# Kernel optimization log

Measured on AMD Instinct MI355X. Metric: run time of the kernel, lower is better.

Reference implementation:

```python
import jax, jax.numpy as jnp
import numpy as np

DN = ('NCHW', 'OIHW', 'NCHW')

def _convlstm_scan(x, W, b):
    """x: [S,B,Cin,H,W]; W: [4*Co, Cin+Co, 3, 3]; b: [4*Co]. Returns all h: [S,B,Co,H,W]."""
    S, B, Cin, H, Wd = x.shape
    Co = W.shape[0] // 4
    h0 = jnp.zeros((B, Co, H, Wd), x.dtype)
    c0 = jnp.zeros((B, Co, H, Wd), x.dtype)

    def step(carry, xt):
        h, c = carry
        z = jax.lax.conv_general_dilated(
            jnp.concatenate([xt, h], axis=1), W,
            window_strides=(1, 1), padding='SAME', dimension_numbers=DN)
        z = z + b[None, :, None, None]
        i, f, o, g = jnp.split(z, 4, axis=1)
        c = jax.nn.sigmoid(f) * c + jax.nn.sigmoid(i) * jnp.tanh(g)
        h = jax.nn.sigmoid(o) * jnp.tanh(c)
        return (h, c), h

    _, outs = jax.lax.scan(step, (h0, c0), x)
    return outs


def setup_inputs() -> dict:
    key = jax.random.key(0)
    k1, k2, k3 = jax.random.split(key, 3)
    S, B, C, H, W = 16, 4, 32, 128, 128
    Co = 32
    x = jax.random.normal(k1, (S, B, C, H, W), dtype=jnp.float32)
    Wf = jax.random.normal(k2, (4 * Co, C + Co, 3, 3), dtype=jnp.float32) * 0.05
    bf = jnp.zeros((4 * Co,), dtype=jnp.float32)
    Wb = jax.random.normal(k3, (4 * Co, C + Co, 3, 3), dtype=jnp.float32) * 0.05
    bb = jnp.zeros((4 * Co,), dtype=jnp.float32)
    return {"x": x, "Wf": Wf, "bf": bf, "Wb": Wb, "bb": bb}


def reference(x, Wf, bf, Wb, bb):
    fwd_outs = _convlstm_scan(x, Wf, bf)            # [S,B,Co,H,W]
    bwd_outs = _convlstm_scan(x[::-1], Wb, bb)      # [S,B,Co,H,W] (time-reversed input)
    # Faithful to source: backward outputs concatenated WITHOUT re-flipping.
    return jnp.concatenate([fwd_outs, bwd_outs], axis=2)  # [S,B,2*Co,H,W]
```

## Files before the change

### kernel.cpp

```cpp
#include <hip/hip_runtime.h>

#define S_ 16
#define B_ 4
#define H_ 128
#define W_ 128
#define HW_ (H_ * W_)
#define NPOS 324
#define TILE_ELEMS (NPOS * 32)

typedef __attribute__((ext_vector_type(8))) _Float16 half8;
typedef __attribute__((ext_vector_type(4))) float f32x4;

__device__ __forceinline__ float sigf(float x) { return 1.f / (1.f + __expf(-x)); }
__device__ __forceinline__ float tanhf_(float x) { return 2.f / (1.f + __expf(-2.f * x)) - 1.f; }

__global__ void prep_pack(const float* __restrict__ Wf, const float* __restrict__ Wb,
                          _Float16* __restrict__ wpk) {
    int id = blockIdx.x * 256 + threadIdx.x;
    if (id >= 18432) return;
    int l = id & 63;
    int nf = (id >> 6) & 7;
    int ks = (id >> 9) % 18;
    int d = id / 9216;
    const float* Wsrc = d ? Wb : Wf;
    int tap = ks >> 1, half = ks & 1;
    int dy = tap / 3, dx = tap - dy * 3;
    int co = nf * 16 + (l & 15);
    _Float16* dst = wpk + (size_t)d * 73728 + ((size_t)(ks * 8 + nf) * 64 + l) * 8;
#pragma unroll
    for (int e = 0; e < 8; ++e) {
        int ci = half * 32 + (l >> 4) * 8 + e;
        dst[e] = (_Float16)Wsrc[((co * 64 + ci) * 3 + dy) * 3 + dx];
    }
}

__global__ void prep_xtiles(const float* __restrict__ x, _Float16* __restrict__ xt) {
    int id = blockIdx.x * 256 + threadIdx.x;
    if (id >= 16 * 4 * 64 * NPOS * 4) return;
    int cb = id & 3;
    int u = id >> 2;
    int pos = u % NPOS;
    int v = u / NPOS;
    int tile = v & 63;
    v >>= 6;
    int b = v & 3;
    int ts = v >> 2;
    int r = pos / 18, cc = pos - r * 18;
    int gy = (tile >> 3) * 16 + r - 1;
    int gx = (tile & 7) * 16 + cc - 1;
    bool inb = ((unsigned)gy < 128u) && ((unsigned)gx < 128u);
    const float* g = x + ((size_t)(ts * 4 + b) * 32 + cb * 8) * HW_ + (size_t)gy * W_ + gx;
    half8 vv;
#pragma unroll
    for (int e = 0; e < 8; ++e)
        vv[e] = inb ? (_Float16)g[e * HW_] : (_Float16)0.f;
    *(half8*)(xt + (size_t)u * 32 + cb * 8) = vv;
}

__device__ __forceinline__ half8 lda(const _Float16* __restrict__ base, int m, int dy,
                                     int dx, int px, int kg, int wq) {
    return *(const half8*)(base + (size_t)(((wq * 4 + m + dy) * 18) + px + dx) * 32 + kg * 8);
}
__device__ __forceinline__ half8 ldb(const _Float16* __restrict__ bw, int ks, int nf, int lane) {
    return *(const half8*)(bw + (size_t)(ks * 8 + nf) * 512 + lane * 8);
}

__global__ __launch_bounds__(256, 2)
void convlstm_step(const _Float16* __restrict__ xtiles,
                   const _Float16* __restrict__ hin,
                   _Float16* __restrict__ hout,
                   const _Float16* __restrict__ wpk,
                   const float* __restrict__ biasf, const float* __restrict__ biasb,
                   float* __restrict__ cst, float* __restrict__ out, int t) {
    const int tile = blockIdx.x;
    const int dirb = blockIdx.y;
    const int dir = dirb >> 2, b = dirb & 3;
    const int ts = dir ? (S_ - 1 - t) : t;

    const _Float16* base_x = xtiles + ((size_t)(ts * 4 + b) * 64 + tile) * TILE_ELEMS;
    const _Float16* base_h = hin + ((size_t)dirb * 64 + tile) * TILE_ELEMS;
    _Float16* hob = hout + (size_t)dirb * 64 * TILE_ELEMS;
    const _Float16* bw = wpk + (size_t)dir * 73728;
    const float* bias = dir ? biasb : biasf;
    float* cbase = cst + (size_t)dirb * 32 * HW_;
    float* outp = out + ((size_t)(t * 4 + b) * 64 + dir * 32) * HW_;

    const int tid = threadIdx.x;
    const int lane = tid & 63, wq = tid >> 6;
    const int px = lane & 15, kg = lane >> 4;

    f32x4 acc[4][8];
#pragma unroll
    for (int m = 0; m < 4; ++m)
#pragma unroll
        for (int nf = 0; nf < 8; ++nf) acc[m][nf] = (f32x4)(0.f);

    if (t == 0) {
#pragma unroll 1
        for (int tap = 0; tap < 9; ++tap) {
            int dy = tap / 3, dx = tap - dy * 3;
            half8 a[4];
#pragma unroll
            for (int m = 0; m < 4; ++m) a[m] = lda(base_x, m, dy, dx, px, kg, wq);
#pragma unroll
            for (int nf = 0; nf < 8; ++nf) {
                half8 bb8 = ldb(bw, tap * 2, nf, lane);
#pragma unroll
                for (int m = 0; m < 4; ++m)
                    acc[m][nf] = __builtin_amdgcn_mfma_f32_16x16x32_f16(a[m], bb8, acc[m][nf], 0, 0, 0);
            }
        }
    } else {
        half8 bcur[8], bnxt[8];
        half8 ax[4], ah[4];
#pragma unroll
        for (int nf = 0; nf < 8; ++nf) bcur[nf] = ldb(bw, 0, nf, lane);
        {
            int dy = 0, dx = 0;
#pragma unroll
            for (int m = 0; m < 4; ++m) ax[m] = lda(base_x, m, dy, dx, px, kg, wq);
        }
#pragma unroll 1
        for (int tap = 0; tap < 9; ++tap) {
            const int dy = tap / 3, dx = tap - dy * 3;
#pragma unroll
            for (int nf = 0; nf < 8; ++nf) bnxt[nf] = ldb(bw, tap * 2 + 1, nf, lane);
#pragma unroll
            for (int m = 0; m < 4; ++m) ah[m] = lda(base_h, m, dy, dx, px, kg, wq);
#pragma unroll
            for (int nf = 0; nf < 8; ++nf)
#pragma unroll
                for (int m = 0; m < 4; ++m)
                    acc[m][nf] = __builtin_amdgcn_mfma_f32_16x16x32_f16(ax[m], bcur[nf], acc[m][nf], 0, 0, 0);
            if (tap < 8) {
                const int tn = tap + 1;
                const int dy2 = tn / 3, dx2 = tn - dy2 * 3;
#pragma unroll
                for (int nf = 0; nf < 8; ++nf) bcur[nf] = ldb(bw, tn * 2, nf, lane);
#pragma unroll
                for (int m = 0; m < 4; ++m) ax[m] = lda(base_x, m, dy2, dx2, px, kg, wq);
            }
#pragma unroll
            for (int nf = 0; nf < 8; ++nf)
#pragma unroll
                for (int m = 0; m < 4; ++m)
                    acc[m][nf] = __builtin_amdgcn_mfma_f32_16x16x32_f16(ah[m], bnxt[nf], acc[m][nf], 0, 0, 0);
        }
    }

    const int q0 = px;
    const int gx0 = (tile & 7) * 16, gy0 = (tile >> 3) * 16;
    const int tx = tile & 7, ty_ = tile >> 3;
    const int lx0 = kg * 4;

    float bI[2], bF[2], bO[2], bG[2];
#pragma unroll
    for (int qs = 0; qs < 2; ++qs) {
        bI[qs] = bias[qs * 16 + q0];
        bF[qs] = bias[32 + qs * 16 + q0];
        bO[qs] = bias[64 + qs * 16 + q0];
        bG[qs] = bias[96 + qs * 16 + q0];
    }
#pragma unroll
    for (int m = 0; m < 4; ++m) {
        const int ly = wq * 4 + m;
        const int gy = gy0 + ly;
#pragma unroll
        for (int qs = 0; qs < 2; ++qs) {
            const int q = qs * 16 + q0;
            f32x4 zi = acc[m][qs], zf = acc[m][2 + qs], zo = acc[m][4 + qs], zg = acc[m][6 + qs];
            size_t off = (size_t)q * HW_ + (size_t)gy * W_ + gx0 + lx0;
            f32x4 cold = (f32x4)(0.f);
            if (t) cold = *(const f32x4*)(cbase + off);
            f32x4 cn, hn;
#pragma unroll
            for (int r = 0; r < 4; ++r) {
                float I = sigf(zi[r] + bI[qs]);
                float F = sigf(zf[r] + bF[qs]);
                float O = sigf(zo[r] + bO[qs]);
                float G = tanhf_(zg[r] + bG[qs]);
                float cnr = F * cold[r] + I * G;
                cn[r] = cnr;
                hn[r] = O * tanhf_(cnr);
            }
            *(f32x4*)(cbase + off) = cn;
            *(f32x4*)(outp + off) = hn;
#pragma unroll
            for (int r = 0; r < 4; ++r) {
                _Float16 hh = (_Float16)hn[r];
                int lx = lx0 + r;
                hob[((size_t)tile) * TILE_ELEMS + (size_t)((ly + 1) * 18 + lx + 1) * 32 + q] = hh;
                bool Le = (lx == 0) && (tx > 0);
                bool Re = (lx == 15) && (tx < 7);
                bool Te = (ly == 0) && (ty_ > 0);
                bool Be = (ly == 15) && (ty_ < 7);
                if (Le) hob[((size_t)tile - 1) * TILE_ELEMS + (size_t)((ly + 1) * 18 + 17) * 32 + q] = hh;
                if (Re) hob[((size_t)tile + 1) * TILE_ELEMS + (size_t)((ly + 1) * 18 + 0) * 32 + q] = hh;
                if (Te) hob[((size_t)tile - 8) * TILE_ELEMS + (size_t)(17 * 18 + lx + 1) * 32 + q] = hh;
                if (Be) hob[((size_t)tile + 8) * TILE_ELEMS + (size_t)(0 * 18 + lx + 1) * 32 + q] = hh;
                if (Te && Le) hob[((size_t)tile - 9) * TILE_ELEMS + (size_t)(17 * 18 + 17) * 32 + q] = hh;
                if (Te && Re) hob[((size_t)tile - 7) * TILE_ELEMS + (size_t)(17 * 18 + 0) * 32 + q] = hh;
                if (Be && Le) hob[((size_t)tile + 7) * TILE_ELEMS + (size_t)(0 * 18 + 17) * 32 + q] = hh;
                if (Be && Re) hob[((size_t)tile + 9) * TILE_ELEMS + (size_t)(0 * 18 + 0) * 32 + q] = hh;
            }
        }
    }
}

extern "C" void kernel_launch(void* const* d_in, const int* in_sizes, int n_in,
                              void* d_out, int out_size, void* d_ws, size_t ws_size,
                              hipStream_t stream) {
    const float* x  = (const float*)d_in[0];
    const float* Wf = (const float*)d_in[1];
    const float* bf = (const float*)d_in[2];
    const float* Wb = (const float*)d_in[3];
    const float* bb = (const float*)d_in[4];
    float* out = (float*)d_out;
    char* ws = (char*)d_ws;

    const size_t OFF_WPK = 0;
    const size_t OFF_XT  = 327680;
    const size_t OFF_H0  = OFF_XT + 84934656;
    const size_t OFF_H1  = OFF_H0 + 10616832;
    const size_t OFF_C   = OFF_H1 + 10616832;

    _Float16* wpk = (_Float16*)(ws + OFF_WPK);
    _Float16* xt  = (_Float16*)(ws + OFF_XT);
    _Float16* hb[2] = { (_Float16*)(ws + OFF_H0), (_Float16*)(ws + OFF_H1) };
    float* cst = (float*)(ws + OFF_C);

    hipMemsetAsync(ws + OFF_H0, 0, 2u * 10616832u, stream);

    prep_pack<<<dim3(72), dim3(256), 0, stream>>>(Wf, Wb, wpk);
    prep_xtiles<<<dim3(20736), dim3(256), 0, stream>>>(x, xt);

    for (int t = 0; t < S_; ++t) {
        convlstm_step<<<dim3(64, 8), dim3(256), 0, stream>>>(
            xt, hb[(t + 1) & 1], hb[t & 1], wpk, bf, bb, cst, out, t);
    }
}
```

Measured before the change: 660.0 us.

## Stage packed weights through double-buffered LDS via direct global-to-LDS loads

In the recurrent path, each wave used to load all eight weight fragments per k-step from global memory into registers. Now each wave loads two fragments per k-step directly into a double-buffered shared-memory tile with global_load_lds, and all waves read them back from LDS. A block barrier is added per k-step, and A-operand loads for the next step are software-pipelined. This cuts redundant global weight traffic and register pressure, at the cost of one __syncthreads per k-step and LDS reads.

```diff
diff --git a/kernel.cpp b/kernel.cpp
--- a/kernel.cpp
+++ b/kernel.cpp
@@ -13,6 +13,12 @@
 
 __device__ __forceinline__ float sigf(float x) { return 1.f / (1.f + __expf(-x)); }
 __device__ __forceinline__ float tanhf_(float x) { return 2.f / (1.f + __expf(-2.f * x)) - 1.f; }
+
+__device__ __forceinline__ void gl2lds16(const _Float16* g, _Float16* l) {
+    __builtin_amdgcn_global_load_lds(
+        (const __attribute__((address_space(1))) unsigned int*)g,
+        (__attribute__((address_space(3))) unsigned int*)l, 16, 0, 0);
+}
 
 __global__ void prep_pack(const float* __restrict__ Wf, const float* __restrict__ Wb,
                           _Float16* __restrict__ wpk) {
@@ -85,6 +91,8 @@
     float* cbase = cst + (size_t)dirb * 32 * HW_;
     float* outp = out + ((size_t)(t * 4 + b) * 64 + dir * 32) * HW_;
 
+    __shared__ alignas(16) _Float16 bsh[2][8][64][8];
+
     const int tid = threadIdx.x;
     const int lane = tid & 63, wq = tid >> 6;
     const int px = lane & 15, kg = lane >> 4;
@@ -111,40 +119,41 @@
             }
         }
     } else {
-        half8 bcur[8], bnxt[8];
-        half8 ax[4], ah[4];
-#pragma unroll
-        for (int nf = 0; nf < 8; ++nf) bcur[nf] = ldb(bw, 0, nf, lane);
+        half8 aP[4], aQ[4];
         {
-            int dy = 0, dx = 0;
-#pragma unroll
-            for (int m = 0; m < 4; ++m) ax[m] = lda(base_x, m, dy, dx, px, kg, wq);
-        }
+            const _Float16* gs = bw + ((size_t)(0 * 8 + wq * 2) * 64 + lane) * 8;
+            gl2lds16(gs, &bsh[0][wq * 2][0][0]);
+            gl2lds16(gs + 512, &bsh[0][wq * 2 + 1][0][0]);
+#pragma unroll
+            for (int m = 0; m < 4; ++m) aP[m] = lda(base_x, m, 0, 0, px, kg, wq);
+        }
+
+        auto body = [&](int ks, half8(&acur)[4], half8(&anxt)[4]) {
+            __syncthreads();
+            if (ks < 17) {
+                const int ksn = ks + 1;
+                const _Float16* gs = bw + ((size_t)(ksn * 8 + wq * 2) * 64 + lane) * 8;
+                gl2lds16(gs, &bsh[ksn & 1][wq * 2][0][0]);
+                gl2lds16(gs + 512, &bsh[ksn & 1][wq * 2 + 1][0][0]);
+                const int tapn = ksn >> 1;
+                const int dyn_ = tapn / 3, dxn = tapn - dyn_ * 3;
+                const _Float16* an = (ksn & 1) ? base_h : base_x;
+#pragma unroll
+                for (int m = 0; m < 4; ++m) anxt[m] = lda(an, m, dyn_, dxn, px, kg, wq);
+            }
+            const _Float16* lb = &bsh[ks & 1][0][0][0];
+#pragma unroll
+            for (int nf = 0; nf < 8; ++nf) {
+                half8 bb8 = *(const half8*)(lb + nf * 512 + lane * 8);
+#pragma unroll
+                for (int m = 0; m < 4; ++m)
+                    acc[m][nf] = __builtin_amdgcn_mfma_f32_16x16x32_f16(acur[m], bb8, acc[m][nf], 0, 0, 0);
+            }
+        };
 #pragma unroll 1
-        for (int tap = 0; tap < 9; ++tap) {
-            const int dy = tap / 3, dx = tap - dy * 3;
-#pragma unroll
-            for (int nf = 0; nf < 8; ++nf) bnxt[nf] = ldb(bw, tap * 2 + 1, nf, lane);
-#pragma unroll
-            for (int m = 0; m < 4; ++m) ah[m] = lda(base_h, m, dy, dx, px, kg, wq);
-#pragma unroll
-            for (int nf = 0; nf < 8; ++nf)
-#pragma unroll
-                for (int m = 0; m < 4; ++m)
-                    acc[m][nf] = __builtin_amdgcn_mfma_f32_16x16x32_f16(ax[m], bcur[nf], acc[m][nf], 0, 0, 0);
-            if (tap < 8) {
-                const int tn = tap + 1;
-                const int dy2 = tn / 3, dx2 = tn - dy2 * 3;
-#pragma unroll
-                for (int nf = 0; nf < 8; ++nf) bcur[nf] = ldb(bw, tn * 2, nf, lane);
-#pragma unroll
-                for (int m = 0; m < 4; ++m) ax[m] = lda(base_x, m, dy2, dx2, px, kg, wq);
-            }
-#pragma unroll
-            for (int nf = 0; nf < 8; ++nf)
-#pragma unroll
-                for (int m = 0; m < 4; ++m)
-                    acc[m][nf] = __builtin_amdgcn_mfma_f32_16x16x32_f16(ah[m], bnxt[nf], acc[m][nf], 0, 0, 0);
+        for (int ks = 0; ks < 18; ks += 2) {
+            body(ks, aP, aQ);
+            body(ks + 1, aQ, aP);
         }
     }
 
```

Result: no change. 649.9 us (-1.5%).
